# Optimization experiments

Measured on AMD Instinct MI355X. Metric: run time of the kernel, lower is better.

Reference implementation:

```python
import jax, jax.numpy as jnp
import numpy as np

N_TV_ITER = 20      # fixed Chambolle iteration count (skimage early-stops via eps; fixed for jit)
TV_WEIGHT = 0.1


def _div(p):
    # negative adjoint of forward-difference gradient (skimage convention)
    d = -(p[0] + p[1])
    d = d.at[1:, :].add(p[0, :-1, :])
    d = d.at[:, 1:].add(p[1, :, :-1])
    return d


def tv_chambolle_2d(image):
    """skimage.restoration.denoise_tv_chambolle on a single 2D image, weight=0.1."""
    tau = 0.25  # 1 / (2 * ndim)

    def step(p, _):
        out = image + _div(p)
        gy = jnp.zeros_like(out).at[:-1, :].set(out[1:, :] - out[:-1, :])
        gx = jnp.zeros_like(out).at[:, :-1].set(out[:, 1:] - out[:, :-1])
        norm = jnp.sqrt(gy * gy + gx * gx)
        g = jnp.stack([gy, gx])
        p = (p - tau * g) / (1.0 + (tau / TV_WEIGHT) * norm)
        return p, None

    p0 = jnp.zeros((2,) + image.shape, image.dtype)
    p, _ = jax.lax.scan(step, p0, None, length=N_TV_ITER)
    return image + _div(p)


def tv_denoise(img):  # [B,C,H,W], vmapped over B*C (replaces the CPU python loop)
    B, C, H, W = img.shape
    out = jax.vmap(tv_chambolle_2d)(img.reshape(B * C, H, W))
    return out.reshape(B, C, H, W)


def conv(x, w, stride=1, groups=1):
    pad = w.shape[2] // 2  # 'same'-style padding for odd kernels, 0 for 1x1
    return jax.lax.conv_general_dilated(
        x, w, (stride, stride), [(pad, pad), (pad, pad)],
        dimension_numbers=('NCHW', 'OIHW', 'NCHW'),
        feature_group_count=groups)


def haar_ll(x):
    # one level of pywt wavedec2('haar') LL band: 0.5 * sum over each 2x2 block
    return 0.5 * (x[..., ::2, ::2] + x[..., ::2, 1::2] + x[..., 1::2, ::2] + x[..., 1::2, 1::2])


def backbone(x, stem_w, dw_pw):
    # stride-32, 1280-channel EfficientNet-B0-style feature extractor
    x = jax.nn.silu(conv(x, stem_w, stride=2))
    for dw, pw in dw_pw:
        x = jax.nn.silu(conv(x, dw, stride=2, groups=dw.shape[0]))
        x = jax.nn.silu(conv(x, pw))
    return x


def setup_inputs() -> dict:
    key = jax.random.key(0)
    ks = jax.random.split(key, 16)
    B, H, W = 4, 512, 512

    def w(k, o, i, kh, kw):
        return jax.random.normal(k, (o, i, kh, kw), jnp.float32) * (1.0 / np.sqrt(i * kh * kw))

    return {
        "img": jax.random.normal(ks[0], (B, 1, H, W), jnp.float32),
        "stem_w": w(ks[1], 32, 1, 3, 3),
        "dw1_w": w(ks[2], 32, 1, 3, 3),  "pw1_w": w(ks[3], 64, 32, 1, 1),
        "dw2_w": w(ks[4], 64, 1, 3, 3),  "pw2_w": w(ks[5], 128, 64, 1, 1),
        "dw3_w": w(ks[6], 128, 1, 3, 3), "pw3_w": w(ks[7], 256, 128, 1, 1),
        "dw4_w": w(ks[8], 256, 1, 3, 3), "pw4_w": w(ks[9], 512, 256, 1, 1),
        "head_w": w(ks[10], 1280, 512, 1, 1),
        "proj_w": w(ks[11], 64, 1280, 1, 1),
        "proj_b": jnp.zeros((64,), jnp.float32),
        "final_w": w(ks[12], 1, 64, 1, 1),
        "final_b": jnp.zeros((1,), jnp.float32),
    }


def reference(img, stem_w, dw1_w, pw1_w, dw2_w, pw2_w, dw3_w, pw3_w, dw4_w, pw4_w,
              head_w, proj_w, proj_b, final_w, final_b):
    B, C, H, W = img.shape
    x = tv_denoise(img)                                     # fused TV Chambolle
    x = backbone(x, stem_w, [(dw1_w, pw1_w), (dw2_w, pw2_w), (dw3_w, pw3_w), (dw4_w, pw4_w)])
    x = jax.nn.silu(conv(x, head_w))                        # [B,1280,H/32,W/32]
    x = conv(x, proj_w) + proj_b[None, :, None, None]       # [B,64,H/32,W/32]
    x = jax.image.resize(x, (B, 64, H, W), method='bilinear')  # align_corners=False semantics
    ll = haar_ll(haar_ll(x))                                # 2-level Haar LL: [B,64,H/4,W/4]
    out = conv(ll, final_w) + final_b[None, :, None, None]  # [B,1,H/4,W/4]
    return out
```

## Files before the change

### kernel.cpp

```cpp
#include <hip/hip_runtime.h>
#include <math.h>

constexpr int BATCH = 4;
constexpr int IMG_H = 512, IMG_W = 512;
constexpr int IMG_HW = IMG_H * IMG_W;
constexpr int PSTR = BATCH * IMG_HW;

constexpr size_t O_PA   = 0;
constexpr size_t O_PB   = O_PA + 2 * (size_t)PSTR;
constexpr size_t O_DEN  = O_PB + 2 * (size_t)PSTR;
constexpr size_t O_A1   = O_DEN + (size_t)PSTR;
constexpr size_t O_A2   = O_A1 + 8388608;
constexpr size_t O_WT1  = O_A2 + 2097152;
constexpr size_t O_WT2  = O_WT1 + 32 * 64;
constexpr size_t O_WT3  = O_WT2 + 64 * 128;
constexpr size_t O_WT4  = O_WT3 + 128 * 256;
constexpr size_t O_WTH  = O_WT4 + 256 * 512;
constexpr size_t O_WCOMB= O_WTH + 512 * 1280;
constexpr size_t O_BCOMB= O_WCOMB + 1280;
constexpr size_t O_S    = O_BCOMB + 4;
constexpr size_t WS_FLOATS = O_S + 1024;

__device__ __forceinline__ float fast_rcp(float x) { return __builtin_amdgcn_rcpf(x); }
__device__ __forceinline__ float fast_sqrt(float x) { return __builtin_amdgcn_sqrtf(x); }
__device__ __forceinline__ float silu_f(float x) {
    float e = __builtin_amdgcn_exp2f(-1.44269504088896f * x);
    return x * fast_rcp(1.0f + e);
}
__device__ __forceinline__ int clampi(int v, int lo, int hi) {
    return v < lo ? lo : (v > hi ? hi : v);
}

template <int NST, bool FIRST, bool LAST>
__global__ __launch_bounds__(512, 8) void tv_reg(const float* __restrict__ img,
                                                 const float* __restrict__ pin,
                                                 float* __restrict__ pout,
                                                 const float* __restrict__ pw1,
                                                 const float* __restrict__ pw2,
                                                 const float* __restrict__ pw3,
                                                 const float* __restrict__ pw4,
                                                 const float* __restrict__ headw,
                                                 const float* __restrict__ projw,
                                                 const float* __restrict__ projb,
                                                 const float* __restrict__ finalw,
                                                 float* __restrict__ ws) {
    constexpr int ROWS = 6, NW = 8, HL = 10, TC = 44, TR = 28;
    constexpr int TVY = 19;
    __shared__ float bndP[2][512], bndO[2][512];

    if constexpr (FIRST) {
        if (blockIdx.y >= TVY) {
            __shared__ float tt[32][33];
            const int tid = threadIdx.x;
            const int pid = ((blockIdx.y - TVY) * 4 + blockIdx.z) * 12 + blockIdx.x;
            for (int t = pid; t < 814; t += 96) {
                const float* src = nullptr; float* dst = nullptr;
                int C = 0, R = 0, tr = 0, tc = 0;
                if (t < 640) {
                    src = headw; dst = ws + O_WTH; R = 1280; C = 512; tr = t >> 4; tc = t & 15;
                } else if (t < 768) {
                    int e = t - 640; src = pw4; dst = ws + O_WT4; R = 512; C = 256; tr = e >> 3; tc = e & 7;
                } else if (t < 800) {
                    int e = t - 768; src = pw3; dst = ws + O_WT3; R = 256; C = 128; tr = e >> 2; tc = e & 3;
                } else if (t < 808) {
                    int e = t - 800; src = pw2; dst = ws + O_WT2; R = 128; C = 64; tr = e >> 1; tc = e & 1;
                } else if (t < 810) {
                    int e = t - 808; src = pw1; dst = ws + O_WT1; R = 64; C = 32; tr = e; tc = 0;
                }
                const int tx = tid & 31, ty = tid >> 5;
                __syncthreads();
                if (src) {
#pragma unroll
                    for (int j = 0; j < 2; ++j)
                        tt[ty + j * 16][tx] =
                            src[(size_t)(tr * 32 + ty + j * 16) * C + tc * 32 + tx];
                }
                __syncthreads();
                if (src) {
#pragma unroll
                    for (int j = 0; j < 2; ++j)
                        dst[(size_t)(tc * 32 + ty + j * 16) * R + tr * 32 + tx] =
                            tt[tx][ty + j * 16];
                } else if (t < 813) {
                    int k = (t - 810) * 512 + tid;
                    if (k < 1280) {
                        float a = 0.0f;
                        for (int ch = 0; ch < 64; ++ch)
                            a = fmaf(finalw[ch], projw[ch * 1280 + k], a);
                        ws[O_WCOMB + k] = a;
                    }
                } else {
                    if (tid == 0) {
                        float a = 0.0f;
                        for (int ch = 0; ch < 64; ++ch) a = fmaf(finalw[ch], projb[ch], a);
                        ws[O_BCOMB] = a;
                    }
                }
            }
            return;
        }
    }

    const int tid = threadIdx.x;
    const int lane = tid & 63, w = tid >> 6;
    const int b = blockIdx.z;
    const int r0 = blockIdx.y * TR, c0 = blockIdx.x * TC;
    const int gj = c0 - HL + lane;
    const int gjc = clampi(gj, 0, 511);
    const int gib = r0 - HL + w * ROWS;
    const float* I = img + b * IMG_HW;
    const bool interior = (r0 - HL >= 1) && (r0 + NW * ROWS - HL <= 511) &&
                          (c0 - HL >= 1) && (c0 + 64 - HL <= 511);

    float rim[ROWS], rp0[ROWS], rp1[ROWS], ro[ROWS];
#pragma unroll
    for (int k = 0; k < ROWS; ++k) {
        int gi = clampi(gib + k, 0, 511);
        rim[k] = I[(gi << 9) + gjc];
    }
    if (!FIRST) {
        const float* P0 = pin + b * IMG_HW;
        const float* P1 = pin + PSTR + b * IMG_HW;
#pragma unroll
        for (int k = 0; k < ROWS; ++k) {
            int gi = clampi(gib + k, 0, 511);
            rp0[k] = P0[(gi << 9) + gjc];
            rp1[k] = P1[(gi << 9) + gjc];
        }
    }
    const bool gjpos = (gj > 0), gjlt = (gj < 511);

    int s0 = 0;
    if (FIRST) {
        bndO[0][tid] = rim[0];
        __syncthreads();
        float odn = (w < NW - 1) ? bndO[0][tid + 64] : 0.0f;
        if (interior) {
#pragma unroll
            for (int k = 0; k < ROWS; ++k) {
                float oR = __shfl_down(rim[k], 1);
                float od = (k < ROWS - 1) ? rim[k + 1] : odn;
                float gy = od - rim[k];
                float gx = oR - rim[k];
                float inv = fast_rcp(fmaf(2.5f, fast_sqrt(fmaf(gy, gy, gx * gx)), 1.0f));
                rp0[k] = -0.25f * gy * inv;
                rp1[k] = -0.25f * gx * inv;
            }
        } else {
#pragma unroll
            for (int k = 0; k < ROWS; ++k) {
                float oR = __shfl_down(rim[k], 1);
                float od = (k < ROWS - 1) ? rim[k + 1] : odn;
                int gi = gib + k;
                float gy = (gi < 511) ? od - rim[k] : 0.0f;
                float gx = gjlt ? oR - rim[k] : 0.0f;
                float inv = fast_rcp(fmaf(2.5f, fast_sqrt(fmaf(gy, gy, gx * gx)), 1.0f));
                rp0[k] = -0.25f * gy * inv;
                rp1[k] = -0.25f * gx * inv;
            }
        }
        s0 = 1;
    }

    for (int s = s0; s < NST; ++s) {
        const int par = s & 1;
        float p1l0 = __shfl_up(rp1[0], 1);
        float partO = rim[0] - rp0[0] - rp1[0];
        if (interior) partO += p1l0;
        else if (gjpos) partO += p1l0;
        bndP[par][tid] = rp0[ROWS - 1];
        bndO[par][tid] = partO;
        __syncthreads();
        float pup0 = (w > 0) ? bndP[par][tid - 64] : 0.0f;
        float odn = (w < NW - 1) ? bndO[par][tid + 64] + rp0[ROWS - 1] : 0.0f;
        if (interior) {
            ro[0] = partO + pup0;
#pragma unroll
            for (int k = 1; k < ROWS; ++k) {
                float p1l = __shfl_up(rp1[k], 1);
                ro[k] = rim[k] - rp0[k] - rp1[k] + rp0[k - 1] + p1l;
            }
#pragma unroll
            for (int k = 0; k < ROWS; ++k) {
                float oR = __shfl_down(ro[k], 1);
                float od = (k < ROWS - 1) ? ro[k + 1] : odn;
                float gy = od - ro[k];
                float gx = oR - ro[k];
                float inv = fast_rcp(fmaf(2.5f, fast_sqrt(fmaf(gy, gy, gx * gx)), 1.0f));
                rp0[k] = (rp0[k] - 0.25f * gy) * inv;
                rp1[k] = (rp1[k] - 0.25f * gx) * inv;
            }
        } else {
            ro[0] = partO + ((gib > 0) ? pup0 : 0.0f);
#pragma unroll
            for (int k = 1; k < ROWS; ++k) {
                float p1l = __shfl_up(rp1[k], 1);
                float o = rim[k] - rp0[k] - rp1[k];
                if (gib + k > 0) o += rp0[k - 1];
                if (gjpos) o += p1l;
                ro[k] = o;
            }
#pragma unroll
            for (int k = 0; k < ROWS; ++k) {
                float oR = __shfl_down(ro[k], 1);
                float od = (k < ROWS - 1) ? ro[k + 1] : odn;
                int gi = gib + k;
                float gy = (gi < 511) ? od - ro[k] : 0.0f;
                float gx = gjlt ? oR - ro[k] : 0.0f;
                float inv = fast_rcp(fmaf(2.5f, fast_sqrt(fmaf(gy, gy, gx * gx)), 1.0f));
                rp0[k] = (rp0[k] - 0.25f * gy) * inv;
                rp1[k] = (rp1[k] - 0.25f * gx) * inv;
            }
        }
    }

    const bool cst = (lane >= HL && lane < HL + TC && gj < 512);
    if (LAST) {
        constexpr int epar = NST & 1;
        bndP[epar][tid] = rp0[ROWS - 1];
        __syncthreads();
        float pup0 = (w > 0) ? bndP[epar][tid - 64] : 0.0f;
        float* D = pout + b * IMG_HW;
#pragma unroll
        for (int k = 0; k < ROWS; ++k) {
            float p1l = __shfl_up(rp1[k], 1);
            int gi = gib + k;
            int rk = w * ROWS + k;
            float o = rim[k] - rp0[k] - rp1[k];
            float pup = (k > 0) ? rp0[k - 1] : pup0;
            if (gi > 0) o += pup;
            if (gjpos) o += p1l;
            if (rk >= HL && rk < HL + TR && cst && gi < 512) D[(gi << 9) + gj] = o;
        }
    } else {
        float* Q0 = pout + b * IMG_HW;
        float* Q1 = pout + PSTR + b * IMG_HW;
#pragma unroll
        for (int k = 0; k < ROWS; ++k) {
            int rk = w * ROWS + k;
            int gi = gib + k;
            if (rk >= HL && rk < HL + TR && cst && gi < 512) {
                Q0[(gi << 9) + gj] = rp0[k];
                Q1[(gi << 9) + gj] = rp1[k];
            }
        }
    }
}

__global__ __launch_bounds__(256) void stem_dw1_pw1(const float* __restrict__ den,
                                                    const float* __restrict__ stemw,
                                                    const float* __restrict__ dw1w,
                                                    const float* __restrict__ pw1T,
                                                    float* __restrict__ out) {
    __shared__ float sDen[35 * 36];
    __shared__ float sStem[8 * 323];
    __shared__ float sDw[32 * 64];
    __shared__ float sW[576];
    __shared__ __align__(16) float sWp[2048];
    const int tid = threadIdx.x;
    const int b = blockIdx.z;
    const int r0 = blockIdx.y * 32, c0 = blockIdx.x * 32;
    const float* D = den + b * IMG_HW;
    for (int e = tid; e < 576; e += 256) sW[e] = (e < 288) ? stemw[e] : dw1w[e - 288];
    for (int e = tid; e < 2048; e += 256) sWp[e] = pw1T[e];
    for (int e = tid; e < 35 * 35; e += 256) {
        int li = e / 35, lj = e % 35;
        int gi = r0 - 3 + li, gjj = c0 - 3 + lj;
        sDen[li * 36 + lj] = (gi >= 0 && gjj >= 0) ? D[(gi << 9) + gjj] : 0.0f;
    }
    __syncthreads();

    for (int g = 0; g < 4; ++g) {
        if (g) __syncthreads();
        for (int e = tid; e < 2312; e += 256) {
            int pos = e >> 3, cl = e & 7;
            int sy = pos / 17, sx = pos % 17;
            int c = 8 * g + cl;
            const float* wc = &sW[c * 9];
            const float* dbase = &sDen[(2 * sy) * 36 + 2 * sx];
            float a = 0.0f;
#pragma unroll
            for (int ky = 0; ky < 3; ++ky)
#pragma unroll
                for (int kx = 0; kx < 3; ++kx)
                    a = fmaf(wc[ky * 3 + kx], dbase[ky * 36 + kx], a);
            sStem[cl * 323 + sy * 19 + sx] = silu_f(a);
        }
        __syncthreads();
        for (int e = tid; e < 512; e += 256) {
            int cl = e >> 6, dy = (e >> 3) & 7, dx = e & 7;
            int c = 8 * g + cl;
            float acc = 0.0f;
#pragma unroll
            for (int ky = 0; ky < 3; ++ky)
#pragma unroll
                for (int kx = 0; kx < 3; ++kx) {
                    int sgy = (r0 >> 1) - 1 + 2 * dy + ky;
                    int sgx = (c0 >> 1) - 1 + 2 * dx + kx;
                    float v = (sgy >= 0 && sgx >= 0)
                        ? sStem[cl * 323 + (2 * dy + ky) * 19 + 2 * dx + kx] : 0.0f;
                    acc = fmaf(sW[288 + c * 9 + ky * 3 + kx], v, acc);
                }
            sDw[c * 64 + (dy << 3) + dx] = silu_f(acc);
        }
    }
    __syncthreads();

    const int px = tid & 63, oc0 = (tid >> 6) * 16;
    float acc[16];
#pragma unroll
    for (int j = 0; j < 16; ++j) acc[j] = 0.0f;
    for (int ic = 0; ic < 32; ++ic) {
        float v = sDw[ic * 64 + px];
        const float* wr = &sWp[ic * 64 + oc0];
#pragma unroll
        for (int q = 0; q < 4; ++q) {
            float4 w4 = *(const float4*)(wr + q * 4);
            acc[q * 4 + 0] = fmaf(v, w4.x, acc[q * 4 + 0]);
            acc[q * 4 + 1] = fmaf(v, w4.y, acc[q * 4 + 1]);
            acc[q * 4 + 2] = fmaf(v, w4.z, acc[q * 4 + 2]);
            acc[q * 4 + 3] = fmaf(v, w4.w, acc[q * 4 + 3]);
        }
    }
    const int gpos = ((r0 >> 2) + (px >> 3)) * 128 + (c0 >> 2) + (px & 7);
    float* ob = out + (size_t)b * 64 * 16384 + (size_t)oc0 * 16384 + gpos;
#pragma unroll
    for (int j = 0; j < 16; ++j) ob[(size_t)j * 16384] = silu_f(acc[j]);
}

template <int C, int HIN>
__global__ __launch_bounds__(256) void dw_kernel(const float* __restrict__ in,
                                                 const float* __restrict__ w,
                                                 float* __restrict__ out) {
    constexpr int HO = HIN / 2;
    int t = blockIdx.x * 256 + threadIdx.x;
    int x = t % HO;
    int y = (t / HO) % HO;
    int c = (t / (HO * HO)) % C;
    int b = t / (HO * HO * C);
    const float* I = in + ((size_t)(b * C + c)) * (HIN * HIN);
    const float* wc = w + c * 9;
    int iy = 2 * y - 1, ix = 2 * x - 1;
    float acc = 0.0f;
#pragma unroll
    for (int ky = 0; ky < 3; ++ky)
#pragma unroll
        for (int kx = 0; kx < 3; ++kx) {
            int yy = iy + ky, xx = ix + kx;
            float vv = (yy >= 0 && xx >= 0) ? I[yy * HIN + xx] : 0.0f;
            acc = fmaf(wc[ky * 3 + kx], vv, acc);
        }
    out[t] = silu_f(acc);
}

template <int C, int HIN>
__global__ __launch_bounds__(256) void dw_reduce2_kernel(const float* __restrict__ part,
                                                         const float* __restrict__ w,
                                                         float* __restrict__ out) {
    constexpr int HO = HIN / 2;
    int t = blockIdx.x * 256 + threadIdx.x;
    int x = t % HO;
    int y = (t / HO) % HO;
    int c = (t / (HO * HO)) % C;
    int b = t / (HO * HO * C);
    const float* Ia = part + ((size_t)(b * C + c)) * (HIN * HIN);
    const float* Ib = Ia + (size_t)BATCH * C * HIN * HIN;
    const float* wc = w + c * 9;
    int iy = 2 * y - 1, ix = 2 * x - 1;
    float acc = 0.0f;
#pragma unroll
    for (int ky = 0; ky < 3; ++ky)
#pragma unroll
        for (int kx = 0; kx < 3; ++kx) {
            int yy = iy + ky, xx = ix + kx;
            float vv = 0.0f;
            if (yy >= 0 && xx >= 0) {
                int o = yy * HIN + xx;
                vv = silu_f(Ia[o] + Ib[o]);
            }
            acc = fmaf(wc[ky * 3 + kx], vv, acc);
        }
    out[t] = silu_f(acc);
}

template <int ICT, int NSIN, int NSPLIT, int OC, bool SILU>
__global__ __launch_bounds__(256) void pw_gemm(const float* __restrict__ in,
                                               const float* __restrict__ wT,
                                               float* __restrict__ out,
                                               int HW) {
    constexpr int KC = 32, TP = 64, TOC = 64, OPT = 4, PPT = 4;
    constexpr int KS = ICT / NSPLIT;
    constexpr int NC = KS / KC;
    constexpr int NOG = TOC / OPT;
    constexpr int PV4 = KC * TP / 4 / 256;
    constexpr int WV4 = KC * TOC / 4 / 256;
    static_assert(KS % KC == 0, "split");
    __shared__ __align__(16) float sPx[2][KC * TP];
    __shared__ __align__(16) float sW[2][KC * TOC];
    const int tid = threadIdx.x;
    const int zb = blockIdx.z;
    const int b = zb / NSPLIT, ks = zb % NSPLIT;
    const int p0 = blockIdx.x * TP;
    const int oc0 = blockIdx.y * TOC;
    const int ocg = tid % NOG, pxg = tid / NOG;
    const size_t instride = (size_t)BATCH * ICT * HW;
    const float* gin0 = in + ((size_t)b * ICT + ks * KS) * HW + p0;
    const float* gw0  = wT + ((size_t)(ks * KS)) * OC + oc0;

    float4 rp[PV4], rw[WV4];
    auto load_chunk = [&](int cc) {
        const float* gin = gin0 + (size_t)cc * KC * HW;
#pragma unroll
        for (int i = 0; i < PV4; ++i) {
            int e = tid + i * 256;
            int row = e / (TP / 4), col = e % (TP / 4);
            const float* base = gin + (size_t)row * HW + col * 4;
            float4 a = *(const float4*)base;
#pragma unroll
            for (int s = 1; s < NSIN; ++s) {
                float4 t4 = *(const float4*)(base + (size_t)s * instride);
                a.x += t4.x; a.y += t4.y; a.z += t4.z; a.w += t4.w;
            }
            if (NSIN > 1) {
                a.x = silu_f(a.x); a.y = silu_f(a.y);
                a.z = silu_f(a.z); a.w = silu_f(a.w);
            }
            rp[i] = a;
        }
        const float* gw = gw0 + (size_t)cc * KC * OC;
#pragma unroll
        for (int i = 0; i < WV4; ++i) {
            int e = tid + i * 256;
            int row = e / (TOC / 4), col = e % (TOC / 4);
            rw[i] = *(const float4*)(gw + (size_t)row * OC + col * 4);
        }
    };
    auto store_chunk = [&](int buf) {
#pragma unroll
        for (int i = 0; i < PV4; ++i) ((float4*)sPx[buf])[tid + i * 256] = rp[i];
#pragma unroll
        for (int i = 0; i < WV4; ++i) ((float4*)sW[buf])[tid + i * 256] = rw[i];
    };

    float acc[OPT][PPT];
#pragma unroll
    for (int o = 0; o < OPT; ++o)
#pragma unroll
        for (int p = 0; p < PPT; ++p) acc[o][p] = 0.0f;

    load_chunk(0);
    store_chunk(0);
    __syncthreads();
    for (int cc = 0; cc < NC; ++cc) {
        if (cc + 1 < NC) load_chunk(cc + 1);
        const int buf = cc & 1;
#pragma unroll 4
        for (int k = 0; k < KC; ++k) {
            float4 pv = *(const float4*)&sPx[buf][k * TP + pxg * PPT];
            float4 wv = *(const float4*)&sW[buf][k * TOC + ocg * OPT];
            float w0 = wv.x, w1 = wv.y, w2 = wv.z, w3 = wv.w;
            acc[0][0] = fmaf(pv.x, w0, acc[0][0]);
            acc[0][1] = fmaf(pv.y, w0, acc[0][1]);
            acc[0][2] = fmaf(pv.z, w0, acc[0][2]);
            acc[0][3] = fmaf(pv.w, w0, acc[0][3]);
            acc[1][0] = fmaf(pv.x, w1, acc[1][0]);
            acc[1][1] = fmaf(pv.y, w1, acc[1][1]);
            acc[1][2] = fmaf(pv.z, w1, acc[1][2]);
            acc[1][3] = fmaf(pv.w, w1, acc[1][3]);
            acc[2][0] = fmaf(pv.x, w2, acc[2][0]);
            acc[2][1] = fmaf(pv.y, w2, acc[2][1]);
            acc[2][2] = fmaf(pv.z, w2, acc[2][2]);
            acc[2][3] = fmaf(pv.w, w2, acc[2][3]);
            acc[3][0] = fmaf(pv.x, w3, acc[3][0]);
            acc[3][1] = fmaf(pv.y, w3, acc[3][1]);
            acc[3][2] = fmaf(pv.z, w3, acc[3][2]);
            acc[3][3] = fmaf(pv.w, w3, acc[3][3]);
        }
        if (cc + 1 < NC) {
            store_chunk((cc + 1) & 1);
            __syncthreads();
        }
    }

    float* ob;
    if (NSPLIT == 1)
        ob = out + ((size_t)(b * OC + oc0 + ocg * OPT)) * HW + p0 + pxg * PPT;
    else
        ob = out + (((size_t)(ks * BATCH + b)) * OC + oc0 + ocg * OPT) * HW + p0 + pxg * PPT;
#pragma unroll
    for (int o = 0; o < OPT; ++o) {
        float4 r;
        r.x = SILU ? silu_f(acc[o][0]) : acc[o][0];
        r.y = SILU ? silu_f(acc[o][1]) : acc[o][1];
        r.z = SILU ? silu_f(acc[o][2]) : acc[o][2];
        r.w = SILU ? silu_f(acc[o][3]) : acc[o][3];
        *(float4*)(ob + (size_t)o * HW) = r;
    }
}

__global__ __launch_bounds__(256) void tail_head(const float* __restrict__ part,
                                                 const float* __restrict__ wcomb,
                                                 const float* __restrict__ bcomb,
                                                 float* __restrict__ s) {
    __shared__ float red[256];
    constexpr size_t PS = (size_t)4 * 1280 * 256;
    int b = blockIdx.x >> 4;
    int px0 = (blockIdx.x & 15) << 4;
    int px = threadIdx.x & 15, kg = threadIdx.x >> 4;
    const float* h0 = part + (size_t)b * 1280 * 256 + px0 + px;
    float acc = 0.0f;
    int k0 = kg * 80;
    for (int k = k0; k < k0 + 80; ++k) {
        size_t off = (size_t)k * 256;
        float v = silu_f(h0[off] + h0[off + PS] + h0[off + 2 * PS] + h0[off + 3 * PS]);
        acc = fmaf(wcomb[k], v, acc);
    }
    red[threadIdx.x] = acc;
    __syncthreads();
    if (threadIdx.x < 16) {
        float a = bcomb[0];
#pragma unroll
        for (int g = 0; g < 16; ++g) a += red[g * 16 + threadIdx.x];
        s[b * 256 + px0 + threadIdx.x] = a;
    }
}

__global__ __launch_bounds__(256) void resize_haar(const float* __restrict__ s,
                                                   const float* __restrict__ finalb,
                                                   float* __restrict__ out) {
    int t = blockIdx.x * 256 + threadIdx.x;
    int c = t & 127, r = (t >> 7) & 127, b = t >> 14;
    const float* S = s + b * 256;
    float acc = 0.0f;
#pragma unroll
    for (int j = 0; j < 4; ++j) {
        float sy = ((4 * r + j) + 0.5f) * (1.0f / 32.0f) - 0.5f;
        int y0 = (int)floorf(sy);
        float fy = sy - (float)y0;
        int ya = y0 < 0 ? 0 : y0;
        int yb = (y0 + 1) > 15 ? 15 : (y0 + 1);
#pragma unroll
        for (int i = 0; i < 4; ++i) {
            float sx = ((4 * c + i) + 0.5f) * (1.0f / 32.0f) - 0.5f;
            int x0 = (int)floorf(sx);
            float fx = sx - (float)x0;
            int xa = x0 < 0 ? 0 : x0;
            int xb = (x0 + 1) > 15 ? 15 : (x0 + 1);
            float v0 = S[ya * 16 + xa] * (1.0f - fx) + S[ya * 16 + xb] * fx;
            float v1 = S[yb * 16 + xa] * (1.0f - fx) + S[yb * 16 + xb] * fx;
            acc += v0 * (1.0f - fy) + v1 * fy;
        }
    }
    out[t] = 0.25f * acc + finalb[0];
}

extern "C" void kernel_launch(void* const* d_in, const int* in_sizes, int n_in,
                              void* d_out, int out_size, void* d_ws, size_t ws_size,
                              hipStream_t stream) {
    if (ws_size < WS_FLOATS * sizeof(float)) return;

    const float* img    = (const float*)d_in[0];
    const float* stem_w = (const float*)d_in[1];
    const float* dw1_w  = (const float*)d_in[2];
    const float* pw1_w  = (const float*)d_in[3];
    const float* dw2_w  = (const float*)d_in[4];
    const float* pw2_w  = (const float*)d_in[5];
    const float* dw3_w  = (const float*)d_in[6];
    const float* pw3_w  = (const float*)d_in[7];
    const float* dw4_w  = (const float*)d_in[8];
    const float* pw4_w  = (const float*)d_in[9];
    const float* head_w = (const float*)d_in[10];
    const float* proj_w = (const float*)d_in[11];
    const float* proj_b = (const float*)d_in[12];
    const float* final_w= (const float*)d_in[13];
    const float* final_b= (const float*)d_in[14];
    float* ws  = (float*)d_ws;
    float* out = (float*)d_out;

    dim3 tvg1(12, 21, 4), tvg2(12, 19, 4);
    tv_reg<10, true,  false><<<tvg1, 512, 0, stream>>>(
        img, img, ws + O_PA,
        pw1_w, pw2_w, pw3_w, pw4_w, head_w, proj_w, proj_b, final_w, ws);
    tv_reg<10, false, true ><<<tvg2, 512, 0, stream>>>(
        img, ws + O_PA, ws + O_DEN,
        nullptr, nullptr, nullptr, nullptr, nullptr, nullptr, nullptr, nullptr, ws);

    stem_dw1_pw1<<<dim3(16, 16, 4), 256, 0, stream>>>(ws + O_DEN, stem_w, dw1_w,
                                                      ws + O_WT1, ws + O_A1);

    dw_kernel<64, 128><<<4096, 256, 0, stream>>>(ws + O_A1, dw2_w, ws + O_A2);
    pw_gemm<64, 1, 2, 128, false><<<dim3(64, 2, 8), 256, 0, stream>>>(ws + O_A2, ws + O_WT2, ws + O_PA, 4096);

    dw_reduce2_kernel<128, 64><<<2048, 256, 0, stream>>>(ws + O_PA, dw3_w, ws + O_A1);
    pw_gemm<128, 1, 2, 256, false><<<dim3(16, 4, 8), 256, 0, stream>>>(ws + O_A1, ws + O_WT3, ws + O_PA, 1024);

    dw_reduce2_kernel<256, 32><<<1024, 256, 0, stream>>>(ws + O_PA, dw4_w, ws + O_A2);
    pw_gemm<256, 1, 4, 512, false><<<dim3(4, 8, 16), 256, 0, stream>>>(ws + O_A2, ws + O_WT4, ws + O_PA, 256);

    pw_gemm<512, 4, 4, 1280, false><<<dim3(4, 20, 16), 256, 0, stream>>>(ws + O_PA, ws + O_WTH, ws + O_A1, 256);
    tail_head<<<64, 256, 0, stream>>>(ws + O_A1, ws + O_WCOMB, ws + O_BCOMB, ws + O_S);

    resize_haar<<<256, 256, 0, stream>>>(ws + O_S, final_b, out);
}
```

Measured before the change: 241.3 us.

## Fuse head GEMM with SiLU and combined projection into one kernel

Replaces the split-K head pointwise GEMM plus the separate tail reduction kernel with a single kernel. It sums the 4 split-K partials of the previous layer on load, applies SiLU, runs the 512x1280 GEMM with double-buffered shared memory, then applies SiLU and the combined projection weights in the epilogue and writes per-OC-tile partial sums. The final reduction over the 20 OC tiles and the bias moves into resize_haar through shared memory. This removes one launch and the large 1280-channel intermediate write and read. In exchange there are fewer blocks with no split-K, so each block runs a longer serial K loop.

Measured after the change: 239.3 us. Within noise of the previous version (-0.8%).

```diff
diff --git a/kernel.cpp b/kernel.cpp
--- a/kernel.cpp
+++ b/kernel.cpp
@@ -498,39 +498,115 @@
     }
 }
 
-__global__ __launch_bounds__(256) void tail_head(const float* __restrict__ part,
-                                                 const float* __restrict__ wcomb,
-                                                 const float* __restrict__ bcomb,
-                                                 float* __restrict__ s) {
-    __shared__ float red[256];
-    constexpr size_t PS = (size_t)4 * 1280 * 256;
-    int b = blockIdx.x >> 4;
-    int px0 = (blockIdx.x & 15) << 4;
-    int px = threadIdx.x & 15, kg = threadIdx.x >> 4;
-    const float* h0 = part + (size_t)b * 1280 * 256 + px0 + px;
-    float acc = 0.0f;
-    int k0 = kg * 80;
-    for (int k = k0; k < k0 + 80; ++k) {
-        size_t off = (size_t)k * 256;
-        float v = silu_f(h0[off] + h0[off + PS] + h0[off + 2 * PS] + h0[off + 3 * PS]);
-        acc = fmaf(wcomb[k], v, acc);
-    }
-    red[threadIdx.x] = acc;
+__global__ __launch_bounds__(256) void head_fused(const float* __restrict__ in,
+                                                  const float* __restrict__ wT,
+                                                  const float* __restrict__ wcomb,
+                                                  float* __restrict__ partial) {
+    constexpr int ICT = 512, KC = 32, TP = 32, TOC = 64, OC = 1280, HW = 256;
+    constexpr int NC = ICT / KC;
+    __shared__ __align__(16) float sPx[2][KC * TP];
+    __shared__ __align__(16) float sW[2][KC * TOC];
+    __shared__ float red[512];
+    const int tid = threadIdx.x;
+    const int b = blockIdx.z;
+    const int p0 = blockIdx.x * TP;
+    const int oc0 = blockIdx.y * TOC;
+    const int ocg = tid & 15, pxg = tid >> 4;
+    const size_t instride = (size_t)BATCH * ICT * HW;
+    const float* gin0 = in + (size_t)b * ICT * HW + p0;
+
+    float4 rp, rw[2];
+    auto load_chunk = [&](int cc) {
+        const float* gin = gin0 + (size_t)cc * KC * HW;
+        {
+            int row = tid >> 3, col = tid & 7;
+            const float* base = gin + (size_t)row * HW + col * 4;
+            float4 a = *(const float4*)base;
+#pragma unroll
+            for (int s = 1; s < 4; ++s) {
+                float4 t4 = *(const float4*)(base + (size_t)s * instride);
+                a.x += t4.x; a.y += t4.y; a.z += t4.z; a.w += t4.w;
+            }
+            a.x = silu_f(a.x); a.y = silu_f(a.y);
+            a.z = silu_f(a.z); a.w = silu_f(a.w);
+            rp = a;
+        }
+        const float* gw = wT + ((size_t)cc * KC) * OC + oc0;
+#pragma unroll
+        for (int i = 0; i < 2; ++i) {
+            int e = tid + i * 256;
+            int row = e >> 4, col = e & 15;
+            rw[i] = *(const float4*)(gw + (size_t)row * OC + col * 4);
+        }
+    };
+    auto store_chunk = [&](int buf) {
+        ((float4*)sPx[buf])[tid] = rp;
+#pragma unroll
+        for (int i = 0; i < 2; ++i) ((float4*)sW[buf])[tid + i * 256] = rw[i];
+    };
+
+    float acc[4][2];
+#pragma unroll
+    for (int o = 0; o < 4; ++o) { acc[o][0] = 0.0f; acc[o][1] = 0.0f; }
+
+    load_chunk(0);
+    store_chunk(0);
     __syncthreads();
-    if (threadIdx.x < 16) {
-        float a = bcomb[0];
-#pragma unroll
-        for (int g = 0; g < 16; ++g) a += red[g * 16 + threadIdx.x];
-        s[b * 256 + px0 + threadIdx.x] = a;
-    }
-}
-
-__global__ __launch_bounds__(256) void resize_haar(const float* __restrict__ s,
+    for (int cc = 0; cc < NC; ++cc) {
+        if (cc + 1 < NC) load_chunk(cc + 1);
+        const int buf = cc & 1;
+#pragma unroll 4
+        for (int k = 0; k < KC; ++k) {
+            float2 pv = *(const float2*)&sPx[buf][k * TP + pxg * 2];
+            float4 wv = *(const float4*)&sW[buf][k * TOC + ocg * 4];
+            acc[0][0] = fmaf(pv.x, wv.x, acc[0][0]);
+            acc[0][1] = fmaf(pv.y, wv.x, acc[0][1]);
+            acc[1][0] = fmaf(pv.x, wv.y, acc[1][0]);
+            acc[1][1] = fmaf(pv.y, wv.y, acc[1][1]);
+            acc[2][0] = fmaf(pv.x, wv.z, acc[2][0]);
+            acc[2][1] = fmaf(pv.y, wv.z, acc[2][1]);
+            acc[3][0] = fmaf(pv.x, wv.w, acc[3][0]);
+            acc[3][1] = fmaf(pv.y, wv.w, acc[3][1]);
+        }
+        if (cc + 1 < NC) {
+            store_chunk((cc + 1) & 1);
+            __syncthreads();
+        }
+    }
+
+    float4 wc4 = *(const float4*)(wcomb + oc0 + ocg * 4);
+#pragma unroll
+    for (int p = 0; p < 2; ++p) {
+        float v = wc4.x * silu_f(acc[0][p]);
+        v = fmaf(wc4.y, silu_f(acc[1][p]), v);
+        v = fmaf(wc4.z, silu_f(acc[2][p]), v);
+        v = fmaf(wc4.w, silu_f(acc[3][p]), v);
+        red[(pxg * 2 + p) * 16 + ocg] = v;
+    }
+    __syncthreads();
+    if (tid < 32) {
+        float a = 0.0f;
+#pragma unroll
+        for (int g = 0; g < 16; ++g) a += red[tid * 16 + g];
+        partial[((size_t)blockIdx.y * 4 + b) * 256 + p0 + tid] = a;
+    }
+}
+
+__global__ __launch_bounds__(256) void resize_haar(const float* __restrict__ partial,
+                                                   const float* __restrict__ bcomb,
                                                    const float* __restrict__ finalb,
                                                    float* __restrict__ out) {
+    __shared__ float sS[256];
     int t = blockIdx.x * 256 + threadIdx.x;
     int c = t & 127, r = (t >> 7) & 127, b = t >> 14;
-    const float* S = s + b * 256;
+    {
+        float a = bcomb[0];
+        const float* P = partial + (size_t)b * 256 + threadIdx.x;
+        for (int y = 0; y < 20; ++y) a += P[(size_t)y * 1024];
+        sS[threadIdx.x] = a;
+    }
+    __syncthreads();
+    const float* S = sS;
     float acc = 0.0f;
 #pragma unroll
     for (int j = 0; j < 4; ++j) {
@@ -597,8 +673,7 @@
     dw_reduce2_kernel<256, 32><<<1024, 256, 0, stream>>>(ws + O_PA, dw4_w, ws + O_A2);
     pw_gemm<256, 1, 4, 512, false><<<dim3(4, 8, 16), 256, 0, stream>>>(ws + O_A2, ws + O_WT4, ws + O_PA, 256);
 
-    pw_gemm<512, 4, 4, 1280, false><<<dim3(4, 20, 16), 256, 0, stream>>>(ws + O_PA, ws + O_WTH, ws + O_A1, 256);
-    tail_head<<<64, 256, 0, stream>>>(ws + O_A1, ws + O_WCOMB, ws + O_BCOMB, ws + O_S);
-
-    resize_haar<<<256, 256, 0, stream>>>(ws + O_S, final_b, out);
-}
+    head_fused<<<dim3(8, 20, 4), 256, 0, stream>>>(ws + O_PA, ws + O_WTH, ws + O_WCOMB, ws + O_A1);
+
+    resize_haar<<<256, 256, 0, stream>>>(ws + O_A1, ws + O_BCOMB, final_b, out);
+}
```
